# Kernel tuning notes

Hardware: AMD Instinct MI355X
Metric: run time of the kernel (lower is better)

The kernel has to match this reference:

```python
import jax, jax.numpy as jnp
import numpy as np

B, H, SQ, SK, D, DV = 2, 16, 2048, 2048, 64, 64
SCALE_FACTOR = 2.0   # non-standard: applied AFTER softmax as 1/scale_factor
DROPOUT_P = 0.1
DROPOUT_KEY = 42     # fixed key -> deterministic dropout mask


def setup_inputs() -> dict:
    key = jax.random.key(0)
    kq, kk, kv = jax.random.split(key, 3)
    return {
        "query": jax.random.normal(kq, (B, H, SQ, D), dtype=jnp.float32),
        "k": jax.random.normal(kk, (H, SK, D), dtype=jnp.float32),
        "v": jax.random.normal(kv, (H, SK, DV), dtype=jnp.float32),
    }


def reference(query, k, v):
    # qk = query @ k^T : [B,H,Sq,Sk]
    qk = jnp.einsum("bhqd,hkd->bhqk", query, k)
    inv_scale = 1.0 / SCALE_FACTOR
    probs = jax.nn.softmax(qk, axis=-1) * inv_scale
    # dropout (train mode, inverted-dropout scaling), deterministic mask
    keep = jax.random.bernoulli(jax.random.key(DROPOUT_KEY), 1.0 - DROPOUT_P, probs.shape)
    probs = jnp.where(keep, probs / (1.0 - DROPOUT_P), 0.0)
    # output = probs @ v : [B,H,Sq,Dv]
    return jnp.einsum("bhqk,hkv->bhqv", probs, v)
```

## Files before the change

kernel.cpp:

```cpp
#include <hip/hip_runtime.h>
#include <stdint.h>
#include <math.h>

namespace {
constexpr int Bb = 2, Hh = 16, SQc = 2048, SKc = 2048, Dc = 64, DVc = 64;
constexpr int TK = 64;

typedef __attribute__((ext_vector_type(8))) short short8;
typedef __attribute__((ext_vector_type(4))) float f32x4;

__device__ __forceinline__ uint32_t rotl_(uint32_t x, int r) {
  return __builtin_amdgcn_alignbit(x, x, 32 - r);
}

__device__ __forceinline__ uint32_t tf_bits(uint32_t ctr) {
  const uint32_t ks1 = 42u, ks2 = 0x1BD11BDAu ^ 42u;
  uint32_t x0 = 0u;
  uint32_t x1 = ctr + ks1;
#define TFR(r) { x0 += x1; x1 = rotl_(x1, r); x1 ^= x0; }
  TFR(13) TFR(15) TFR(26) TFR(6)
  x0 += ks1; x1 += ks2 + 1u;
  TFR(17) TFR(29) TFR(16) TFR(24)
  x0 += ks2; x1 += 0u + 2u;
  TFR(13) TFR(15) TFR(26) TFR(6)
  x0 += 0u; x1 += ks1 + 3u;
  TFR(17) TFR(29) TFR(16) TFR(24)
  x0 += ks1; x1 += ks2 + 4u;
  TFR(13) TFR(15) TFR(26) TFR(6)
  x0 += ks2; x1 += 0u + 5u;
#undef TFR
  return x0 ^ x1;
}

__device__ __forceinline__ uint32_t f2bf_u(float x) {
  uint32_t u = __float_as_uint(x);
  u += 0x7FFFu + ((u >> 16) & 1u);
  return u >> 16;
}
__device__ __forceinline__ uint32_t bfround(float x) {
  uint32_t u = __float_as_uint(x);
  return u + 0x7FFFu + ((u >> 16) & 1u);
}

__device__ __forceinline__ void gl_lds16(const void* g, void* l) {
  __builtin_amdgcn_global_load_lds(
      (const __attribute__((address_space(1))) unsigned int*)g,
      (__attribute__((address_space(3))) unsigned int*)l, 16, 0, 0);
}
}

__global__ __launch_bounds__(256) void prep_kernel(
    const float* __restrict__ k, const float* __restrict__ v,
    unsigned short* __restrict__ Khg, unsigned short* __restrict__ Klg,
    unsigned short* __restrict__ Vtg) {
  __shared__ float Vs[64 * 65];
  const int t = threadIdx.x;
  const int h = blockIdx.x >> 5;
  const int kt = blockIdx.x & 31;
  const size_t src = ((size_t)h * SKc + kt * 64) * Dc;
  const size_t tb = (size_t)(h * 32 + kt) * 4096;
#pragma unroll
  for (int i = 0; i < 4; ++i) {
    int idx = t + 256 * i;
    int row = idx >> 4, d0 = (idx & 15) << 2;
    float4 kv = *(const float4*)(k + src + row * Dc + d0);
    uint32_t hx = f2bf_u(kv.x), hy = f2bf_u(kv.y), hz = f2bf_u(kv.z), hw = f2bf_u(kv.w);
    uint32_t lx = f2bf_u(kv.x - __uint_as_float(hx << 16));
    uint32_t ly = f2bf_u(kv.y - __uint_as_float(hy << 16));
    uint32_t lz = f2bf_u(kv.z - __uint_as_float(hz << 16));
    uint32_t lw = f2bf_u(kv.w - __uint_as_float(hw << 16));
    int phys = row * 64 + (((d0 >> 3) ^ (row & 7)) << 3) + (d0 & 7);
    *(ushort4*)(Khg + tb + phys) =
        make_ushort4((unsigned short)hx, (unsigned short)hy, (unsigned short)hz, (unsigned short)hw);
    *(ushort4*)(Klg + tb + phys) =
        make_ushort4((unsigned short)lx, (unsigned short)ly, (unsigned short)lz, (unsigned short)lw);
    float4 vv = *(const float4*)(v + src + row * Dc + d0);
    *(float4*)(&Vs[row * 65 + d0]) = vv;
  }
  __syncthreads();
  const int dv = t >> 2;
  const int j0 = (t & 3) << 1;
#pragma unroll
  for (int g = 0; g < 2; ++g) {
    int chunk = j0 + g;
    unsigned short tmp[8];
#pragma unroll
    for (int s = 0; s < 8; ++s)
      tmp[s] = (unsigned short)f2bf_u(Vs[(chunk * 8 + s) * 65 + dv]);
    *(short8*)(Vtg + tb + dv * 64 + ((chunk ^ (dv & 7)) << 3)) = *(const short8*)tmp;
  }
}

__global__ __launch_bounds__(256, 4) void attn_main(
    const float* __restrict__ q, const unsigned short* __restrict__ Khg,
    const unsigned short* __restrict__ Klg, const unsigned short* __restrict__ Vtg,
    float* __restrict__ out) {
  __shared__ __align__(16) unsigned short stag[12288];

  const int t = threadIdx.x;
  const int lane = t & 63;
  const int w = t >> 6;
  const int lm = lane & 15;
  const int quad = lane >> 4;

  const int vid = (blockIdx.x & 7) * 128 + (blockIdx.x >> 3);
  const int qt = vid & 31;
  const int h = (vid >> 5) & 15;
  const int b = vid >> 9;
  const int qrow = qt * 64 + w * 16 + lm;

  short8 qh[2], ql[2];
  {
    const float* qp = q + (((size_t)(b * Hh + h)) * SQc + qrow) * Dc;
#pragma unroll
    for (int c = 0; c < 2; ++c) {
#pragma unroll
      for (int j2 = 0; j2 < 2; ++j2) {
        float4 x = *(const float4*)(qp + c * 32 + quad * 8 + j2 * 4);
        float xs[4] = {x.x, x.y, x.z, x.w};
#pragma unroll
        for (int j = 0; j < 4; ++j) {
          uint32_t hb = f2bf_u(xs[j]);
          float lo = xs[j] - __uint_as_float(hb << 16);
          qh[c][j2 * 4 + j] = (short)hb;
          ql[c][j2 * 4 + j] = (short)f2bf_u(lo);
        }
      }
    }
  }

  const char* kh_t = (const char*)Khg + (size_t)(h * 32) * 8192;
  const char* kl_t = (const char*)Klg + (size_t)(h * 32) * 8192;
  const char* vt_t = (const char*)Vtg + (size_t)(h * 32) * 8192;

  f32x4 acc[4] = {{0.f, 0.f, 0.f, 0.f}, {0.f, 0.f, 0.f, 0.f},
                  {0.f, 0.f, 0.f, 0.f}, {0.f, 0.f, 0.f, 0.f}};
  float l_i = 0.f;

  const int e = lm & 7;
  const int a0s = lm * 64 + ((quad ^ e) << 3);
  const int a1s = lm * 64 + (((quad + 4) ^ e) << 3);

  const int pa0 = ((quad & 1) * 32 + lm) << 2;
  const int pa1 = pa0 + 64;
  const uint32_t sel = (quad >= 2) ? 0x07060302u : 0x05040100u;

  uint32_t ctile = ((uint32_t)((b * Hh + h) * SQc + qrow)) * (uint32_t)SKc + (uint32_t)(quad * 4);

#pragma unroll 1
  for (int kt = 0; kt < 32; ++kt, ctile += TK) {
    __syncthreads();
    {
      const size_t tile = (size_t)kt * 8192;
#pragma unroll
      for (int r = 0; r < 2; ++r) {
        int off = r * 4096 + w * 1024 + lane * 16;
        gl_lds16(kh_t + tile + off, (char*)stag + off);
        gl_lds16(kl_t + tile + off, (char*)stag + 8192 + off);
        gl_lds16(vt_t + tile + off, (char*)stag + 16384 + off);
      }
    }
    __syncthreads();

#pragma unroll
    for (int c = 0; c < 2; ++c) {
      f32x4 s0 = {0.f, 0.f, 0.f, 0.f}, s1 = {0.f, 0.f, 0.f, 0.f};
#pragma unroll
      for (int d = 0; d < 2; ++d) {
        const int ad = (d == 0) ? a0s : a1s;
        short8 kh0 = *(const short8*)&stag[ad + (2 * c) * 1024];
        short8 kl0 = *(const short8*)&stag[ad + (2 * c) * 1024 + 4096];
        s0 = __builtin_amdgcn_mfma_f32_16x16x32_bf16(kh0, qh[d], s0, 0, 0, 0);
        s0 = __builtin_amdgcn_mfma_f32_16x16x32_bf16(kl0, qh[d], s0, 0, 0, 0);
        s0 = __builtin_amdgcn_mfma_f32_16x16x32_bf16(kh0, ql[d], s0, 0, 0, 0);
        short8 kh1 = *(const short8*)&stag[ad + (2 * c + 1) * 1024];
        short8 kl1 = *(const short8*)&stag[ad + (2 * c + 1) * 1024 + 4096];
        s1 = __builtin_amdgcn_mfma_f32_16x16x32_bf16(kh1, qh[d], s1, 0, 0, 0);
        s1 = __builtin_amdgcn_mfma_f32_16x16x32_bf16(kl1, qh[d], s1, 0, 0, 0);
        s1 = __builtin_amdgcn_mfma_f32_16x16x32_bf16(kh1, ql[d], s1, 0, 0, 0);
      }

      uint32_t pkc[4];
#pragma unroll
      for (int r = 0; r < 4; ++r) {
        float p0 = __expf(s0[r]);
        float p1 = __expf(s1[r]);
        l_i += p0 + p1;
        uint32_t b0 = tf_bits(ctile + (uint32_t)(c * 32 + r));
        uint32_t b1 = tf_bits(ctile + (uint32_t)(c * 32 + 16 + r));
        uint32_t u0 = (b0 < 0xE6666600u) ? bfround(p0) : 0u;
        uint32_t u1 = (b1 < 0xE6666600u) ? bfround(p1) : 0u;
        pkc[r] = __builtin_amdgcn_perm(u1, u0, 0x07060302u);
      }

      short8 pb;
      {
        uint32_t e0 = (uint32_t)__builtin_amdgcn_ds_bpermute(pa0, (int)pkc[0]);
        uint32_t e1 = (uint32_t)__builtin_amdgcn_ds_bpermute(pa0, (int)pkc[1]);
        uint32_t e2 = (uint32_t)__builtin_amdgcn_ds_bpermute(pa0, (int)pkc[2]);
        uint32_t e3 = (uint32_t)__builtin_amdgcn_ds_bpermute(pa0, (int)pkc[3]);
        uint32_t f0 = (uint32_t)__builtin_amdgcn_ds_bpermute(pa1, (int)pkc[0]);
        uint32_t f1 = (uint32_t)__builtin_amdgcn_ds_bpermute(pa1, (int)pkc[1]);
        uint32_t f2 = (uint32_t)__builtin_amdgcn_ds_bpermute(pa1, (int)pkc[2]);
        uint32_t f3 = (uint32_t)__builtin_amdgcn_ds_bpermute(pa1, (int)pkc[3]);
        uint32_t w0 = __builtin_amdgcn_perm(e1, e0, sel);
        uint32_t w1 = __builtin_amdgcn_perm(e3, e2, sel);
        uint32_t w2 = __builtin_amdgcn_perm(f1, f0, sel);
        uint32_t w3 = __builtin_amdgcn_perm(f3, f2, sel);
        uint32_t tmp[4] = {w0, w1, w2, w3};
        pb = *(const short8*)tmp;
      }

      {
        const int ac = (c == 0) ? a0s : a1s;
#pragma unroll
        for (int nb = 0; nb < 4; ++nb) {
          short8 vb = *(const short8*)&stag[ac + nb * 1024 + 8192];
          acc[nb] = __builtin_amdgcn_mfma_f32_16x16x32_bf16(vb, pb, acc[nb], 0, 0, 0);
        }
      }
    }
  }

  l_i += __shfl_xor(l_i, 16);
  l_i += __shfl_xor(l_i, 32);
  float sc = (0.5f / 0.9f) / l_i;
  float* op = out + (((size_t)(b * Hh + h)) * SQc + qrow) * DVc;
#pragma unroll
  for (int nb = 0; nb < 4; ++nb) {
    float4 o = make_float4(acc[nb][0] * sc, acc[nb][1] * sc,
                           acc[nb][2] * sc, acc[nb][3] * sc);
    *(float4*)(op + nb * 16 + quad * 4) = o;
  }
}

extern "C" void kernel_launch(void* const* d_in, const int* in_sizes, int n_in,
                              void* d_out, int out_size, void* d_ws, size_t ws_size,
                              hipStream_t stream) {
  const float* q = (const float*)d_in[0];
  const float* k = (const float*)d_in[1];
  const float* v = (const float*)d_in[2];
  float* out = (float*)d_out;
  unsigned short* Khg = (unsigned short*)d_ws;
  unsigned short* Klg = Khg + (size_t)Hh * SKc * Dc;
  unsigned short* Vtg = Klg + (size_t)Hh * SKc * Dc;
  prep_kernel<<<dim3(Hh * 32), 256, 0, stream>>>(k, v, Khg, Klg, Vtg);
  attn_main<<<dim3(Bb * Hh * (SQc / 64)), 256, 0, stream>>>(q, Khg, Klg, Vtg, out);
}
```

Before: 364.7 us.

## Split key range across two warp groups per block with LDS reduction

Doubles the block to 512 threads. Each pair of wave groups processes half of the key tiles for the same 64 query rows, each group using its own LDS staging buffer. Partial accumulators and row sums are combined through shared memory at the end. The goal is more parallelism and latency hiding per block, since there is no running max to rescale. The cost is extra LDS use, an end-of-kernel reduction, and higher register pressure under launch_bounds(512,6).

```diff
diff --git a/kernel.cpp b/kernel.cpp
--- a/kernel.cpp
+++ b/kernel.cpp
@@ -91,23 +91,25 @@
   }
 }
 
-__global__ __launch_bounds__(256, 4) void attn_main(
+__global__ __launch_bounds__(512, 6) void attn_main(
     const float* __restrict__ q, const unsigned short* __restrict__ Khg,
     const unsigned short* __restrict__ Klg, const unsigned short* __restrict__ Vtg,
     float* __restrict__ out) {
-  __shared__ __align__(16) unsigned short stag[12288];
+  __shared__ __align__(16) unsigned short stag[2][12288];
 
   const int t = threadIdx.x;
   const int lane = t & 63;
   const int w = t >> 6;
   const int lm = lane & 15;
   const int quad = lane >> 4;
+  const int khalf = w & 1;
+  const int qsub = w >> 1;
 
   const int vid = (blockIdx.x & 7) * 128 + (blockIdx.x >> 3);
   const int qt = vid & 31;
   const int h = (vid >> 5) & 15;
   const int b = vid >> 9;
-  const int qrow = qt * 64 + w * 16 + lm;
+  const int qrow = qt * 64 + qsub * 16 + lm;
 
   short8 qh[2], ql[2];
   {
@@ -132,6 +134,7 @@
   const char* kh_t = (const char*)Khg + (size_t)(h * 32) * 8192;
   const char* kl_t = (const char*)Klg + (size_t)(h * 32) * 8192;
   const char* vt_t = (const char*)Vtg + (size_t)(h * 32) * 8192;
+  unsigned short* sb = &stag[khalf][0];
 
   f32x4 acc[4] = {{0.f, 0.f, 0.f, 0.f}, {0.f, 0.f, 0.f, 0.f},
                   {0.f, 0.f, 0.f, 0.f}, {0.f, 0.f, 0.f, 0.f}};
@@ -145,19 +148,21 @@
   const int pa1 = pa0 + 64;
   const uint32_t sel = (quad >= 2) ? 0x07060302u : 0x05040100u;
 
-  uint32_t ctile = ((uint32_t)((b * Hh + h) * SQc + qrow)) * (uint32_t)SKc + (uint32_t)(quad * 4);
+  uint32_t ctile = ((uint32_t)((b * Hh + h) * SQc + qrow)) * (uint32_t)SKc +
+                   (uint32_t)(khalf * 16 * TK + quad * 4);
 
 #pragma unroll 1
-  for (int kt = 0; kt < 32; ++kt, ctile += TK) {
+  for (int i = 0; i < 16; ++i, ctile += TK) {
+    const int kt = khalf * 16 + i;
     __syncthreads();
     {
       const size_t tile = (size_t)kt * 8192;
 #pragma unroll
       for (int r = 0; r < 2; ++r) {
-        int off = r * 4096 + w * 1024 + lane * 16;
-        gl_lds16(kh_t + tile + off, (char*)stag + off);
-        gl_lds16(kl_t + tile + off, (char*)stag + 8192 + off);
-        gl_lds16(vt_t + tile + off, (char*)stag + 16384 + off);
+        int off = r * 4096 + qsub * 1024 + lane * 16;
+        gl_lds16(kh_t + tile + off, (char*)sb + off);
+        gl_lds16(kl_t + tile + off, (char*)sb + 8192 + off);
+        gl_lds16(vt_t + tile + off, (char*)sb + 16384 + off);
       }
     }
     __syncthreads();
@@ -168,13 +173,13 @@
 #pragma unroll
       for (int d = 0; d < 2; ++d) {
         const int ad = (d == 0) ? a0s : a1s;
-        short8 kh0 = *(const short8*)&stag[ad + (2 * c) * 1024];
-        short8 kl0 = *(const short8*)&stag[ad + (2 * c) * 1024 + 4096];
+        short8 kh0 = *(const short8*)&sb[ad + (2 * c) * 1024];
+        short8 kl0 = *(const short8*)&sb[ad + (2 * c) * 1024 + 4096];
         s0 = __builtin_amdgcn_mfma_f32_16x16x32_bf16(kh0, qh[d], s0, 0, 0, 0);
         s0 = __builtin_amdgcn_mfma_f32_16x16x32_bf16(kl0, qh[d], s0, 0, 0, 0);
         s0 = __builtin_amdgcn_mfma_f32_16x16x32_bf16(kh0, ql[d], s0, 0, 0, 0);
-        short8 kh1 = *(const short8*)&stag[ad + (2 * c + 1) * 1024];
-        short8 kl1 = *(const short8*)&stag[ad + (2 * c + 1) * 1024 + 4096];
+        short8 kh1 = *(const short8*)&sb[ad + (2 * c + 1) * 1024];
+        short8 kl1 = *(const short8*)&sb[ad + (2 * c + 1) * 1024 + 4096];
         s1 = __builtin_amdgcn_mfma_f32_16x16x32_bf16(kh1, qh[d], s1, 0, 0, 0);
         s1 = __builtin_amdgcn_mfma_f32_16x16x32_bf16(kl1, qh[d], s1, 0, 0, 0);
         s1 = __builtin_amdgcn_mfma_f32_16x16x32_bf16(kh1, ql[d], s1, 0, 0, 0);
@@ -215,7 +220,7 @@
         const int ac = (c == 0) ? a0s : a1s;
 #pragma unroll
         for (int nb = 0; nb < 4; ++nb) {
-          short8 vb = *(const short8*)&stag[ac + nb * 1024 + 8192];
+          short8 vb = *(const short8*)&sb[ac + nb * 1024 + 8192];
           acc[nb] = __builtin_amdgcn_mfma_f32_16x16x32_bf16(vb, pb, acc[nb], 0, 0, 0);
         }
       }
@@ -224,13 +229,28 @@
 
   l_i += __shfl_xor(l_i, 16);
   l_i += __shfl_xor(l_i, 32);
-  float sc = (0.5f / 0.9f) / l_i;
-  float* op = out + (((size_t)(b * Hh + h)) * SQc + qrow) * DVc;
-#pragma unroll
-  for (int nb = 0; nb < 4; ++nb) {
-    float4 o = make_float4(acc[nb][0] * sc, acc[nb][1] * sc,
-                           acc[nb][2] * sc, acc[nb][3] * sc);
-    *(float4*)(op + nb * 16 + quad * 4) = o;
+
+  float (*Lacc)[16][72] = (float(*)[16][72])&stag[0][0];
+  float* Ll = (float*)((char*)&stag[0][0] + 18432);
+  __syncthreads();
+  if (khalf == 1) {
+#pragma unroll
+    for (int nb = 0; nb < 4; ++nb)
+      *(f32x4*)&Lacc[qsub][lm][nb * 16 + quad * 4] = acc[nb];
+    if (quad == 0) Ll[qsub * 16 + lm] = l_i;
+  }
+  __syncthreads();
+  if (khalf == 0) {
+    float lt = l_i + Ll[qsub * 16 + lm];
+    float sc = (0.5f / 0.9f) / lt;
+    float* op = out + (((size_t)(b * Hh + h)) * SQc + qrow) * DVc;
+#pragma unroll
+    for (int nb = 0; nb < 4; ++nb) {
+      f32x4 other = *(const f32x4*)&Lacc[qsub][lm][nb * 16 + quad * 4];
+      float4 o = make_float4((acc[nb][0] + other[0]) * sc, (acc[nb][1] + other[1]) * sc,
+                             (acc[nb][2] + other[2]) * sc, (acc[nb][3] + other[3]) * sc);
+      *(float4*)(op + nb * 16 + quad * 4) = o;
+    }
   }
 }
 
@@ -245,5 +265,5 @@
   unsigned short* Klg = Khg + (size_t)Hh * SKc * Dc;
   unsigned short* Vtg = Klg + (size_t)Hh * SKc * Dc;
   prep_kernel<<<dim3(Hh * 32), 256, 0, stream>>>(k, v, Khg, Klg, Vtg);
-  attn_main<<<dim3(Bb * Hh * (SQc / 64)), 256, 0, stream>>>(q, Khg, Klg, Vtg, out);
-}
+  attn_main<<<dim3(Bb * Hh * (SQc / 64)), 512, 0, stream>>>(q, Khg, Klg, Vtg, out);
+}
```

Result: no change. 361.1 us (-1.0%).
